# Optimization experiments

Hardware: AMD Instinct MI355X
Metric: run time of the kernel (lower is better)

## Reference

```python
import jax, jax.numpy as jnp
import numpy as np

N_ENT, N_USR, N_ITEM, N_REL, N_CLS, N_FAC, D = 100000, 4096, 8192, 32, 3, 8, 128
N_EDGES, NNZ = 800000, 204800


def setup_inputs() -> dict:
    key = jax.random.key(0)
    ks = jax.random.split(key, 15)
    return {
        "entity_emb": jax.random.normal(ks[0], (N_ENT, D), jnp.float32),
        "item_emb": jax.random.normal(ks[1], (N_ITEM, D), jnp.float32),
        "user_emb": jax.random.normal(ks[2], (N_USR, D), jnp.float32),
        "latent_emb": jax.random.normal(ks[3], (N_FAC, D), jnp.float32),
        "relation_emb": jax.random.normal(ks[4], (N_REL, D), jnp.float32),
        "edge_index": jax.random.randint(ks[5], (2, N_EDGES), 0, N_ENT, jnp.int32),
        "edge_type": jax.random.randint(ks[6], (N_EDGES,), 0, N_REL, jnp.int32),
        "edge_imp": jax.random.uniform(ks[7], (N_EDGES,), jnp.float32),
        "inter_rows": jax.random.randint(ks[8], (NNZ,), 0, N_USR, jnp.int32),
        "inter_cols": jax.random.randint(ks[9], (NNZ,), 0, N_ENT, jnp.int32),
        "inter_vals": jax.random.uniform(ks[10], (NNZ,), jnp.float32),
        "disen_weight_att": jax.random.normal(ks[11], (N_FAC, N_REL), jnp.float32),
        "ent_rel_w": jax.random.normal(ks[12], (N_REL, D), jnp.float32),
        "usr_cls_w": jax.random.normal(ks[13], (N_CLS, D), jnp.float32),
        "inter_cls_mat": jax.random.normal(ks[14], (N_CLS, N_USR, N_ITEM), jnp.float32),
    }


def reference(entity_emb, item_emb, user_emb, latent_emb, relation_emb,
              edge_index, edge_type, edge_imp, inter_rows, inter_cols,
              inter_vals, disen_weight_att, ent_rel_w, usr_cls_w, inter_cls_mat):
    n_entities = entity_emb.shape[0]
    n_users = user_emb.shape[0]
    head, tail = edge_index[0], edge_index[1]

    # --- entity aggregation, e_mode='att_imp' ---
    # per-entity attention over relations: [n_ent, n_rel]
    ent_rel_att = jax.nn.softmax(entity_emb @ relation_emb.T, axis=1)
    mess_att = ent_rel_att[head, edge_type][:, None]              # [E,1]
    message_score = relation_emb[edge_type] * mess_att * edge_imp[:, None]  # [E,D]
    message = entity_emb[tail] * message_score                    # [E,D]
    entity_agg = jax.ops.segment_sum(message, head, num_segments=n_entities)

    # --- user aggregation, u_mode='inter_cls' ---
    # sparse interact_mat @ entity_emb via COO gather + segment_sum
    user_agg = jax.ops.segment_sum(entity_emb[inter_cols] * inter_vals[:, None],
                                   inter_rows, num_segments=n_users)
    user_cls_att = jax.nn.softmax(user_emb @ usr_cls_w.T, axis=1)  # [U,C]
    item_emb_2 = item_emb * relation_emb.sum(axis=0, keepdims=True)  # [I,D]
    # stack_c(inter_cls_mat[c] @ item_emb_2).transpose(0,1) -> [U,C,D]
    disen_weight = jnp.einsum('cui,id->ucd', inter_cls_mat, item_emb_2)
    user_agg = user_agg + (disen_weight * user_cls_att[:, :, None]).sum(axis=1)

    return entity_agg, user_agg
```

## Files before the change

kernel.cpp:

```cpp
#include <hip/hip_runtime.h>

#define N_ENT   100000
#define N_USR   4096
#define N_ITEM  8192
#define N_REL   32
#define N_CLS   3
#define DD      128
#define N_EDGES 800000
#define NNZ     204800

#define CAP_E   64
#define CAP_U   128

typedef __attribute__((ext_vector_type(8))) short short8;
typedef __attribute__((ext_vector_type(4))) float f32x4;

static __device__ __forceinline__ unsigned short f2bf(float x) {
    unsigned int u = __builtin_bit_cast(unsigned int, x);
    u = (u + 0x7fffu + ((u >> 16) & 1u)) >> 16;
    return (unsigned short)u;
}
static __device__ __forceinline__ float bflo(unsigned int v) {
    return __uint_as_float(v << 16);
}
static __device__ __forceinline__ float bfhi(unsigned int v) {
    return __uint_as_float(v & 0xffff0000u);
}

#define ZB  ((N_ENT + N_USR + 255) / 256)
#define EAB ((N_ENT + 255) / 256)

__global__ __launch_bounds__(256) void k_prep(const float* __restrict__ ent,
                                              const float* __restrict__ rel,
                                              float* __restrict__ att,
                                              unsigned short* __restrict__ entbf,
                                              unsigned short* __restrict__ relbf,
                                              int* __restrict__ cnt,
                                              const float* __restrict__ item,
                                              unsigned short* __restrict__ Bt,
                                              const float* __restrict__ usr,
                                              const float* __restrict__ w,
                                              float* __restrict__ uatt) {
    __shared__ float smem[N_REL * DD];
    int bx = blockIdx.x;

    if (bx < ZB) {
        int i = bx * 256 + threadIdx.x;
        if (i < N_ENT + N_USR) cnt[i] = 0;
        return;
    }
    bx -= ZB;

    if (bx < EAB) {
        for (int i = threadIdx.x; i < N_REL * DD; i += 256) smem[i] = rel[i];
        __syncthreads();
        if (bx == 0) {
            for (int i = threadIdx.x; i < N_REL * DD; i += 256)
                relbf[i] = f2bf(smem[i]);
        }
        int e = bx * 256 + threadIdx.x;
        if (e >= N_ENT) return;
        const float4* row = (const float4*)(ent + (size_t)e * DD);
        unsigned short* brow = entbf + (size_t)e * DD;
        float acc[N_REL];
#pragma unroll
        for (int r = 0; r < N_REL; ++r) acc[r] = 0.f;
        for (int dq = 0; dq < DD / 4; ++dq) {
            float4 v = row[dq];
            ushort4 bv;
            bv.x = f2bf(v.x); bv.y = f2bf(v.y); bv.z = f2bf(v.z); bv.w = f2bf(v.w);
            *(ushort4*)(brow + dq * 4) = bv;
#pragma unroll
            for (int r = 0; r < N_REL; ++r) {
                float4 ww = *(const float4*)&smem[r * DD + dq * 4];
                acc[r] += v.x * ww.x + v.y * ww.y + v.z * ww.z + v.w * ww.w;
            }
        }
        float m = acc[0];
#pragma unroll
        for (int r = 1; r < N_REL; ++r) m = fmaxf(m, acc[r]);
        float s = 0.f;
#pragma unroll
        for (int r = 0; r < N_REL; ++r) { acc[r] = __expf(acc[r] - m); s += acc[r]; }
        float inv = 1.f / s;
        float* o = att + (size_t)e * N_REL;
#pragma unroll
        for (int r = 0; r < N_REL; ++r) o[r] = acc[r] * inv;
        return;
    }
    bx -= EAB;

    if (bx < 1024) {
        float (*tile)[33] = (float(*)[33])smem;
        float* ssum = smem + 32 * 33;
        const int b2 = bx & 255, by = bx >> 8;
        const int tx = threadIdx.x & 31, ty = threadIdx.x >> 5;
        const int i0 = b2 * 32, d0 = by * 32;
        if (threadIdx.x < 32) {
            float s = 0.f;
            for (int r = 0; r < N_REL; ++r) s += rel[r * DD + d0 + threadIdx.x];
            ssum[threadIdx.x] = s;
        }
#pragma unroll
        for (int rr = 0; rr < 4; ++rr)
            tile[ty + 8 * rr][tx] = item[(size_t)(i0 + ty + 8 * rr) * DD + d0 + tx];
        __syncthreads();
#pragma unroll
        for (int rr = 0; rr < 4; ++rr) {
            int d = d0 + ty + 8 * rr;
            Bt[(size_t)d * N_ITEM + i0 + tx] = f2bf(tile[tx][ty + 8 * rr] * ssum[ty + 8 * rr]);
        }
        return;
    }
    bx -= 1024;

    {
        for (int i = threadIdx.x; i < N_CLS * DD; i += 256) smem[i] = w[i];
        __syncthreads();
        int u = bx * 256 + threadIdx.x;
        const float4* row = (const float4*)(usr + (size_t)u * DD);
        float acc[3] = {0.f, 0.f, 0.f};
        for (int dq = 0; dq < DD / 4; ++dq) {
            float4 v = row[dq];
#pragma unroll
            for (int c = 0; c < 3; ++c) {
                float4 ww = *(const float4*)&smem[c * DD + dq * 4];
                acc[c] += v.x * ww.x + v.y * ww.y + v.z * ww.z + v.w * ww.w;
            }
        }
        float m = fmaxf(acc[0], fmaxf(acc[1], acc[2]));
        float s = 0.f;
#pragma unroll
        for (int c = 0; c < 3; ++c) { acc[c] = __expf(acc[c] - m); s += acc[c]; }
        float inv = 1.f / s;
#pragma unroll
        for (int c = 0; c < 3; ++c) uatt[u * 3 + c] = acc[c] * inv;
    }
}

#define BM 64
#define BK 32
#define SPLITK 16
#define KCH (N_ITEM / SPLITK)
#define PLANE ((long long)N_USR * N_ITEM)
#define GEMM_BLOCKS ((N_USR / BM) * SPLITK)
#define SCAT_BLOCKS ((N_EDGES + 255) / 256)

__global__ __launch_bounds__(256) void k_node2(const float* __restrict__ icm,
                                               const unsigned short* __restrict__ Bt,
                                               const float* __restrict__ uatt,
                                               float* __restrict__ part,
                                               const int* __restrict__ eidx,
                                               const int* __restrict__ etyp,
                                               const float* __restrict__ eimp,
                                               const int* __restrict__ irow,
                                               const int* __restrict__ icol,
                                               const float* __restrict__ ival,
                                               int* __restrict__ cnt,
                                               int2* __restrict__ pack_e,
                                               int2* __restrict__ pack_u) {
    __shared__ unsigned short smem[BM * 40 + DD * 40];

    if (blockIdx.x < GEMM_BLOCKS) {
        unsigned short (*sA)[40] = (unsigned short(*)[40])smem;
        unsigned short (*sB)[40] = (unsigned short(*)[40])(smem + BM * 40);

        const int t  = threadIdx.x;
        const int m0 = (blockIdx.x & 63) * BM;
        const int ky = blockIdx.x >> 6;
        const long long k0b = (long long)ky * KCH;

        const int ua = t >> 3;
        const int qa = t & 7;
        const float a00 = uatt[(m0 + ua) * 3 + 0];
        const float a01 = uatt[(m0 + ua) * 3 + 1];
        const float a02 = uatt[(m0 + ua) * 3 + 2];
        const float a10 = uatt[(m0 + ua + 32) * 3 + 0];
        const float a11 = uatt[(m0 + ua + 32) * 3 + 1];
        const float a12 = uatt[(m0 + ua + 32) * 3 + 2];

        const int db = t >> 2;
        const int qb = t & 3;

        const int lane = t & 63;
        const int wv = t >> 6;
        const int wm = wv >> 1, wn = wv & 1;
        const int la = lane & 15, lb = lane >> 4;

        f32x4 acc[2][4];
#pragma unroll
        for (int mi = 0; mi < 2; ++mi)
#pragma unroll
            for (int ni = 0; ni < 4; ++ni) {
                f32x4 z = {0.f, 0.f, 0.f, 0.f};
                acc[mi][ni] = z;
            }

        float4 rA0[3], rA1[3];
        short8 rB0, rB1;
        {
            const long long base0 = (long long)(m0 + ua) * N_ITEM + k0b + qa * 4;
            rA0[0] = *(const float4*)(icm + base0);
            rA0[1] = *(const float4*)(icm + base0 + PLANE);
            rA0[2] = *(const float4*)(icm + base0 + 2 * PLANE);
            const long long base1 = base0 + 32ll * N_ITEM;
            rA1[0] = *(const float4*)(icm + base1);
            rA1[1] = *(const float4*)(icm + base1 + PLANE);
            rA1[2] = *(const float4*)(icm + base1 + 2 * PLANE);
            const unsigned short* g0 = Bt + (long long)db * N_ITEM + k0b + qb * 8;
            rB0 = *(const short8*)g0;
            rB1 = *(const short8*)(g0 + 64ll * N_ITEM);
        }

        for (int kk = 0; kk < KCH; kk += BK) {
            __syncthreads();
            {
                ushort4 p;
                p.x = f2bf(a00 * rA0[0].x + a01 * rA0[1].x + a02 * rA0[2].x);
                p.y = f2bf(a00 * rA0[0].y + a01 * rA0[1].y + a02 * rA0[2].y);
                p.z = f2bf(a00 * rA0[0].z + a01 * rA0[1].z + a02 * rA0[2].z);
                p.w = f2bf(a00 * rA0[0].w + a01 * rA0[1].w + a02 * rA0[2].w);
                *(ushort4*)(&sA[ua][0] + qa * 4) = p;
                p.x = f2bf(a10 * rA1[0].x + a11 * rA1[1].x + a12 * rA1[2].x);
                p.y = f2bf(a10 * rA1[0].y + a11 * rA1[1].y + a12 * rA1[2].y);
                p.z = f2bf(a10 * rA1[0].z + a11 * rA1[1].z + a12 * rA1[2].z);
                p.w = f2bf(a10 * rA1[0].w + a11 * rA1[1].w + a12 * rA1[2].w);
                *(ushort4*)(&sA[ua + 32][0] + qa * 4) = p;
                *(short8*)(&sB[db][0] + qb * 8) = rB0;
                *(short8*)(&sB[db + 64][0] + qb * 8) = rB1;
            }
            __syncthreads();

            if (kk + BK < KCH) {
                const long long k0 = k0b + kk + BK;
                const long long base0 = (long long)(m0 + ua) * N_ITEM + k0 + qa * 4;
                rA0[0] = *(const float4*)(icm + base0);
                rA0[1] = *(const float4*)(icm + base0 + PLANE);
                rA0[2] = *(const float4*)(icm + base0 + 2 * PLANE);
                const long long base1 = base0 + 32ll * N_ITEM;
                rA1[0] = *(const float4*)(icm + base1);
                rA1[1] = *(const float4*)(icm + base1 + PLANE);
                rA1[2] = *(const float4*)(icm + base1 + 2 * PLANE);
                const unsigned short* g0 = Bt + (long long)db * N_ITEM + k0 + qb * 8;
                rB0 = *(const short8*)g0;
                rB1 = *(const short8*)(g0 + 64ll * N_ITEM);
            }

            short8 af[2], bfr[4];
#pragma unroll
            for (int mi = 0; mi < 2; ++mi)
                af[mi] = *(const short8*)(&sA[wm * 32 + mi * 16 + la][0] + lb * 8);
#pragma unroll
            for (int ni = 0; ni < 4; ++ni)
                bfr[ni] = *(const short8*)(&sB[wn * 64 + ni * 16 + la][0] + lb * 8);
#pragma unroll
            for (int mi = 0; mi < 2; ++mi)
#pragma unroll
                for (int ni = 0; ni < 4; ++ni)
                    acc[mi][ni] = __builtin_amdgcn_mfma_f32_16x16x32_bf16(
                        af[mi], bfr[ni], acc[mi][ni], 0, 0, 0);
        }

        float* pbase = part + (size_t)ky * ((size_t)N_USR * DD);
#pragma unroll
        for (int mi = 0; mi < 2; ++mi)
#pragma unroll
            for (int ni = 0; ni < 4; ++ni)
#pragma unroll
                for (int r = 0; r < 4; ++r) {
                    int row = m0 + wm * 32 + mi * 16 + lb * 4 + r;
                    int col = wn * 64 + ni * 16 + la;
                    pbase[(size_t)row * DD + col] = acc[mi][ni][r];
                }
    } else {
        int i = (blockIdx.x - GEMM_BLOCKS) * 256 + threadIdx.x;
        if (i < N_EDGES) {
            int h = eidx[i], tl = eidx[N_EDGES + i], r = etyp[i];
            int p = atomicAdd(&cnt[h], 1);
            if (p < CAP_E) {
                int2 pk;
                pk.x = tl | (r << 24);
                pk.y = __float_as_int(eimp[i]);
                pack_e[(size_t)h * CAP_E + p] = pk;
            }
        }
        if (i < NNZ) {
            int u = irow[i];
            int p = atomicAdd(&cnt[N_ENT + u], 1);
            if (p < CAP_U) {
                int2 pk;
                pk.x = icol[i];
                pk.y = __float_as_int(ival[i]);
                pack_u[(size_t)u * CAP_U + p] = pk;
            }
        }
    }
}

#define EDGE_BLOCKS (N_ENT / 16)
#define USER_BLOCKS (N_USR / 4)

__global__ __launch_bounds__(256) void k_node3(const unsigned short* __restrict__ entbf,
                                               const unsigned short* __restrict__ relbf,
                                               const float* __restrict__ att,
                                               const int2* __restrict__ pack_e,
                                               const int2* __restrict__ pack_u,
                                               const int* __restrict__ cnt,
                                               const float* __restrict__ part,
                                               float* __restrict__ out_ent,
                                               float* __restrict__ out_usr) {
    const int lane = threadIdx.x & 63;

    if (blockIdx.x < EDGE_BLOCKS) {
        const int wid = blockIdx.x * 4 + (threadIdx.x >> 6);
#pragma unroll
        for (int hh = 0; hh < 4; ++hh) {
            const int h = wid * 4 + hh;
            const int n = min(cnt[h], CAP_E);
            const float attv = att[(size_t)h * N_REL + (lane & 31)];
            const int2* seg = pack_e + (size_t)h * CAP_E;
            float ax = 0.f, ay = 0.f;
            for (int j = 0; j < n; j += 8) {
                int2 pk[8];
#pragma unroll
                for (int k = 0; k < 8; ++k) pk[k] = seg[min(j + k, n - 1)];
                unsigned int bv[8], rv[8];
                float sc[8];
#pragma unroll
                for (int k = 0; k < 8; ++k) {
                    int r = ((unsigned)pk[k].x) >> 24;
                    float s = __shfl(attv, r, 64) * __int_as_float(pk[k].y);
                    sc[k] = (j + k < n) ? s : 0.f;
                    bv[k] = ((const unsigned int*)(entbf + (size_t)(pk[k].x & 0xFFFFFF) * DD))[lane];
                    rv[k] = ((const unsigned int*)(relbf + (size_t)r * DD))[lane];
                }
#pragma unroll
                for (int k = 0; k < 8; ++k) {
                    ax = fmaf(bflo(rv[k]) * bflo(bv[k]), sc[k], ax);
                    ay = fmaf(bfhi(rv[k]) * bfhi(bv[k]), sc[k], ay);
                }
            }
            float2 o; o.x = ax; o.y = ay;
            ((float2*)(out_ent + (size_t)h * DD))[lane] = o;
        }
    } else {
        const int u = (blockIdx.x - EDGE_BLOCKS) * 4 + (threadIdx.x >> 6);
        const int n = min(cnt[N_ENT + u], CAP_U);
        const int2* seg = pack_u + (size_t)u * CAP_U;
        float ax = 0.f, ay = 0.f;
        for (int j = 0; j < n; j += 8) {
            int2 pk[8];
#pragma unroll
            for (int k = 0; k < 8; ++k) pk[k] = seg[min(j + k, n - 1)];
            unsigned int bv[8];
            float sc[8];
#pragma unroll
            for (int k = 0; k < 8; ++k) {
                sc[k] = (j + k < n) ? __int_as_float(pk[k].y) : 0.f;
                bv[k] = ((const unsigned int*)(entbf + (size_t)pk[k].x * DD))[lane];
            }
#pragma unroll
            for (int k = 0; k < 8; ++k) {
                ax = fmaf(bflo(bv[k]), sc[k], ax);
                ay = fmaf(bfhi(bv[k]), sc[k], ay);
            }
        }
#pragma unroll
        for (int k = 0; k < SPLITK; ++k) {
            float2 p = ((const float2*)(part + (size_t)k * N_USR * DD + (size_t)u * DD))[lane];
            ax += p.x;
            ay += p.y;
        }
        float2 o; o.x = ax; o.y = ay;
        ((float2*)(out_usr + (size_t)u * DD))[lane] = o;
    }
}

static constexpr size_t algn(size_t x) { return (x + 255) & ~(size_t)255; }

extern "C" void kernel_launch(void* const* d_in, const int* in_sizes, int n_in,
                              void* d_out, int out_size, void* d_ws, size_t ws_size,
                              hipStream_t stream) {
    const float* ent  = (const float*)d_in[0];
    const float* item = (const float*)d_in[1];
    const float* usr  = (const float*)d_in[2];
    const float* rel  = (const float*)d_in[4];
    const int*   eidx = (const int*)d_in[5];
    const int*   etyp = (const int*)d_in[6];
    const float* eimp = (const float*)d_in[7];
    const int*   irow = (const int*)d_in[8];
    const int*   icol = (const int*)d_in[9];
    const float* ival = (const float*)d_in[10];
    const float* uclw = (const float*)d_in[13];
    const float* icm  = (const float*)d_in[14];

    float* out_ent = (float*)d_out;
    float* out_usr = out_ent + (size_t)N_ENT * DD;

    char* w = (char*)d_ws;
    size_t o = 0;
    float* ws_att  = (float*)(w + o);  o = algn(o + (size_t)N_ENT * N_REL * 4);
    float* ws_uatt = (float*)(w + o);  o = algn(o + (size_t)N_USR * N_CLS * 4);
    unsigned short* ws_Bt    = (unsigned short*)(w + o); o = algn(o + (size_t)DD * N_ITEM * 2);
    unsigned short* ws_entbf = (unsigned short*)(w + o); o = algn(o + (size_t)N_ENT * DD * 2);
    unsigned short* ws_relbf = (unsigned short*)(w + o); o = algn(o + (size_t)N_REL * DD * 2);
    int*  ws_cnt   = (int*)(w + o);  o = algn(o + (size_t)(N_ENT + N_USR) * 4);
    int2* pack_e   = (int2*)(w + o); o = algn(o + (size_t)N_ENT * CAP_E * 8);
    int2* pack_u   = (int2*)(w + o); o = algn(o + (size_t)N_USR * CAP_U * 8);
    float* part    = (float*)(w + o); o = algn(o + (size_t)SPLITK * N_USR * DD * 4);

    (void)in_sizes; (void)n_in; (void)ws_size; (void)out_size;

    k_prep<<<ZB + EAB + 1024 + 16, 256, 0, stream>>>(ent, rel, ws_att, ws_entbf, ws_relbf,
                                                     ws_cnt, item, ws_Bt, usr, uclw, ws_uatt);
    k_node2<<<GEMM_BLOCKS + SCAT_BLOCKS, 256, 0, stream>>>(icm, ws_Bt, ws_uatt, part,
                                                           eidx, etyp, eimp, irow, icol, ival,
                                                           ws_cnt, pack_e, pack_u);
    k_node3<<<EDGE_BLOCKS + USER_BLOCKS, 256, 0, stream>>>(ws_entbf, ws_relbf, ws_att,
                                                           pack_e, pack_u, ws_cnt, part,
                                                           out_ent, out_usr);
}
```

Baseline: 313.8 us.

## Move entity attention prep into GEMM kernel and vectorize edge gather

The per-entity relation-softmax and bf16 conversion blocks move from the prep kernel into the GEMM/scatter kernel. They now run concurrently with the memory-bound split-K GEMM instead of ahead of it, which shortens the serial prep stage. The edge aggregation in k_node3 is also restructured so each 16-lane group loads 16-byte chunks of two edges per step, and partial sums are reduced across groups with xor shuffles. The shared-memory footprint of k_node2 grows to 16KB, which may reduce GEMM block occupancy.

```diff
diff --git a/kernel.cpp b/kernel.cpp
--- a/kernel.cpp
+++ b/kernel.cpp
@@ -28,20 +28,15 @@
 }
 
 #define ZB  ((N_ENT + N_USR + 255) / 256)
-#define EAB ((N_ENT + 255) / 256)
-
-__global__ __launch_bounds__(256) void k_prep(const float* __restrict__ ent,
-                                              const float* __restrict__ rel,
-                                              float* __restrict__ att,
-                                              unsigned short* __restrict__ entbf,
-                                              unsigned short* __restrict__ relbf,
-                                              int* __restrict__ cnt,
-                                              const float* __restrict__ item,
-                                              unsigned short* __restrict__ Bt,
-                                              const float* __restrict__ usr,
-                                              const float* __restrict__ w,
-                                              float* __restrict__ uatt) {
-    __shared__ float smem[N_REL * DD];
+
+__global__ __launch_bounds__(256) void k_prep_light(const float* __restrict__ rel,
+                                                    int* __restrict__ cnt,
+                                                    const float* __restrict__ item,
+                                                    unsigned short* __restrict__ Bt,
+                                                    const float* __restrict__ usr,
+                                                    const float* __restrict__ w,
+                                                    float* __restrict__ uatt) {
+    __shared__ float smem[32 * 33 + 32];
     int bx = blockIdx.x;
 
     if (bx < ZB) {
@@ -50,45 +45,6 @@
         return;
     }
     bx -= ZB;
-
-    if (bx < EAB) {
-        for (int i = threadIdx.x; i < N_REL * DD; i += 256) smem[i] = rel[i];
-        __syncthreads();
-        if (bx == 0) {
-            for (int i = threadIdx.x; i < N_REL * DD; i += 256)
-                relbf[i] = f2bf(smem[i]);
-        }
-        int e = bx * 256 + threadIdx.x;
-        if (e >= N_ENT) return;
-        const float4* row = (const float4*)(ent + (size_t)e * DD);
-        unsigned short* brow = entbf + (size_t)e * DD;
-        float acc[N_REL];
-#pragma unroll
-        for (int r = 0; r < N_REL; ++r) acc[r] = 0.f;
-        for (int dq = 0; dq < DD / 4; ++dq) {
-            float4 v = row[dq];
-            ushort4 bv;
-            bv.x = f2bf(v.x); bv.y = f2bf(v.y); bv.z = f2bf(v.z); bv.w = f2bf(v.w);
-            *(ushort4*)(brow + dq * 4) = bv;
-#pragma unroll
-            for (int r = 0; r < N_REL; ++r) {
-                float4 ww = *(const float4*)&smem[r * DD + dq * 4];
-                acc[r] += v.x * ww.x + v.y * ww.y + v.z * ww.z + v.w * ww.w;
-            }
-        }
-        float m = acc[0];
-#pragma unroll
-        for (int r = 1; r < N_REL; ++r) m = fmaxf(m, acc[r]);
-        float s = 0.f;
-#pragma unroll
-        for (int r = 0; r < N_REL; ++r) { acc[r] = __expf(acc[r] - m); s += acc[r]; }
-        float inv = 1.f / s;
-        float* o = att + (size_t)e * N_REL;
-#pragma unroll
-        for (int r = 0; r < N_REL; ++r) o[r] = acc[r] * inv;
-        return;
-    }
-    bx -= EAB;
 
     if (bx < 1024) {
         float (*tile)[33] = (float(*)[33])smem;
@@ -144,12 +100,18 @@
 #define KCH (N_ITEM / SPLITK)
 #define PLANE ((long long)N_USR * N_ITEM)
 #define GEMM_BLOCKS ((N_USR / BM) * SPLITK)
+#define EAB ((N_ENT + 255) / 256)
 #define SCAT_BLOCKS ((N_EDGES + 255) / 256)
 
 __global__ __launch_bounds__(256) void k_node2(const float* __restrict__ icm,
                                                const unsigned short* __restrict__ Bt,
                                                const float* __restrict__ uatt,
                                                float* __restrict__ part,
+                                               const float* __restrict__ ent,
+                                               const float* __restrict__ rel,
+                                               float* __restrict__ att,
+                                               unsigned short* __restrict__ entbf,
+                                               unsigned short* __restrict__ relbf,
                                                const int* __restrict__ eidx,
                                                const int* __restrict__ etyp,
                                                const float* __restrict__ eimp,
@@ -159,9 +121,10 @@
                                                int* __restrict__ cnt,
                                                int2* __restrict__ pack_e,
                                                int2* __restrict__ pack_u) {
-    __shared__ unsigned short smem[BM * 40 + DD * 40];
+    __shared__ float smemf[N_REL * DD];
 
     if (blockIdx.x < GEMM_BLOCKS) {
+        unsigned short* smem = (unsigned short*)smemf;
         unsigned short (*sA)[40] = (unsigned short(*)[40])smem;
         unsigned short (*sB)[40] = (unsigned short(*)[40])(smem + BM * 40);
 
@@ -272,8 +235,50 @@
                     int col = wn * 64 + ni * 16 + la;
                     pbase[(size_t)row * DD + col] = acc[mi][ni][r];
                 }
-    } else {
-        int i = (blockIdx.x - GEMM_BLOCKS) * 256 + threadIdx.x;
+        return;
+    }
+
+    if (blockIdx.x < GEMM_BLOCKS + EAB) {
+        int bx = blockIdx.x - GEMM_BLOCKS;
+        for (int i = threadIdx.x; i < N_REL * DD; i += 256) smemf[i] = rel[i];
+        __syncthreads();
+        if (bx == 0) {
+            for (int i = threadIdx.x; i < N_REL * DD; i += 256)
+                relbf[i] = f2bf(smemf[i]);
+        }
+        int e = bx * 256 + threadIdx.x;
+        if (e >= N_ENT) return;
+        const float4* row = (const float4*)(ent + (size_t)e * DD);
+        unsigned short* brow = entbf + (size_t)e * DD;
+        float acc[N_REL];
+#pragma unroll
+        for (int r = 0; r < N_REL; ++r) acc[r] = 0.f;
+        for (int dq = 0; dq < DD / 4; ++dq) {
+            float4 v = row[dq];
+            ushort4 bv;
+            bv.x = f2bf(v.x); bv.y = f2bf(v.y); bv.z = f2bf(v.z); bv.w = f2bf(v.w);
+            *(ushort4*)(brow + dq * 4) = bv;
+#pragma unroll
+            for (int r = 0; r < N_REL; ++r) {
+                float4 ww = *(const float4*)&smemf[r * DD + dq * 4];
+                acc[r] += v.x * ww.x + v.y * ww.y + v.z * ww.z + v.w * ww.w;
+            }
+        }
+        float m = acc[0];
+#pragma unroll
+        for (int r = 1; r < N_REL; ++r) m = fmaxf(m, acc[r]);
+        float s = 0.f;
+#pragma unroll
+        for (int r = 0; r < N_REL; ++r) { acc[r] = __expf(acc[r] - m); s += acc[r]; }
+        float inv = 1.f / s;
+        float* o = att + (size_t)e * N_REL;
+#pragma unroll
+        for (int r = 0; r < N_REL; ++r) o[r] = acc[r] * inv;
+        return;
+    }
+
+    {
+        int i = (blockIdx.x - GEMM_BLOCKS - EAB) * 256 + threadIdx.x;
         if (i < N_EDGES) {
             int h = eidx[i], tl = eidx[N_EDGES + i], r = etyp[i];
             int p = atomicAdd(&cnt[h], 1);
@@ -313,35 +318,55 @@
 
     if (blockIdx.x < EDGE_BLOCKS) {
         const int wid = blockIdx.x * 4 + (threadIdx.x >> 6);
-#pragma unroll
+        const int l15 = lane & 15;
+        const int grp = lane >> 4;
+#pragma unroll 1
         for (int hh = 0; hh < 4; ++hh) {
             const int h = wid * 4 + hh;
             const int n = min(cnt[h], CAP_E);
             const float attv = att[(size_t)h * N_REL + (lane & 31)];
             const int2* seg = pack_e + (size_t)h * CAP_E;
-            float ax = 0.f, ay = 0.f;
+            float acc[8];
+#pragma unroll
+            for (int e = 0; e < 8; ++e) acc[e] = 0.f;
             for (int j = 0; j < n; j += 8) {
-                int2 pk[8];
-#pragma unroll
-                for (int k = 0; k < 8; ++k) pk[k] = seg[min(j + k, n - 1)];
-                unsigned int bv[8], rv[8];
-                float sc[8];
-#pragma unroll
-                for (int k = 0; k < 8; ++k) {
-                    int r = ((unsigned)pk[k].x) >> 24;
-                    float s = __shfl(attv, r, 64) * __int_as_float(pk[k].y);
-                    sc[k] = (j + k < n) ? s : 0.f;
-                    bv[k] = ((const unsigned int*)(entbf + (size_t)(pk[k].x & 0xFFFFFF) * DD))[lane];
-                    rv[k] = ((const unsigned int*)(relbf + (size_t)r * DD))[lane];
+                const int e0 = j + grp, e1 = j + 4 + grp;
+                int2 p0 = seg[min(e0, n - 1)];
+                int2 p1 = seg[min(e1, n - 1)];
+                const int r0 = ((unsigned)p0.x) >> 24;
+                const int r1 = ((unsigned)p1.x) >> 24;
+                float s0 = __shfl(attv, r0, 64) * __int_as_float(p0.y);
+                float s1 = __shfl(attv, r1, 64) * __int_as_float(p1.y);
+                s0 = (e0 < n) ? s0 : 0.f;
+                s1 = (e1 < n) ? s1 : 0.f;
+                uint4 b0 = ((const uint4*)(entbf + (size_t)(p0.x & 0xFFFFFF) * DD))[l15];
+                uint4 b1 = ((const uint4*)(entbf + (size_t)(p1.x & 0xFFFFFF) * DD))[l15];
+                uint4 v0 = ((const uint4*)(relbf + (size_t)r0 * DD))[l15];
+                uint4 v1 = ((const uint4*)(relbf + (size_t)r1 * DD))[l15];
+                const unsigned* bp0 = (const unsigned*)&b0;
+                const unsigned* bp1 = (const unsigned*)&b1;
+                const unsigned* vp0 = (const unsigned*)&v0;
+                const unsigned* vp1 = (const unsigned*)&v1;
+#pragma unroll
+                for (int q = 0; q < 4; ++q) {
+                    acc[2 * q]     = fmaf(bflo(bp0[q]) * bflo(vp0[q]), s0, acc[2 * q]);
+                    acc[2 * q + 1] = fmaf(bfhi(bp0[q]) * bfhi(vp0[q]), s0, acc[2 * q + 1]);
+                    acc[2 * q]     = fmaf(bflo(bp1[q]) * bflo(vp1[q]), s1, acc[2 * q]);
+                    acc[2 * q + 1] = fmaf(bfhi(bp1[q]) * bfhi(vp1[q]), s1, acc[2 * q + 1]);
                 }
-#pragma unroll
-                for (int k = 0; k < 8; ++k) {
-                    ax = fmaf(bflo(rv[k]) * bflo(bv[k]), sc[k], ax);
-                    ay = fmaf(bfhi(rv[k]) * bfhi(bv[k]), sc[k], ay);
-                }
-            }
-            float2 o; o.x = ax; o.y = ay;
-            ((float2*)(out_ent + (size_t)h * DD))[lane] = o;
+            }
+#pragma unroll
+            for (int e = 0; e < 8; ++e) {
+                acc[e] += __shfl_xor(acc[e], 16, 64);
+                acc[e] += __shfl_xor(acc[e], 32, 64);
+            }
+            if (lane < 16) {
+                float4 o0 = {acc[0], acc[1], acc[2], acc[3]};
+                float4 o1 = {acc[4], acc[5], acc[6], acc[7]};
+                float4* dst = (float4*)(out_ent + (size_t)h * DD) + l15 * 2;
+                dst[0] = o0;
+                dst[1] = o1;
+            }
         }
     } else {
         const int u = (blockIdx.x - EDGE_BLOCKS) * 4 + (threadIdx.x >> 6);
@@ -411,11 +436,11 @@
 
     (void)in_sizes; (void)n_in; (void)ws_size; (void)out_size;
 
-    k_prep<<<ZB + EAB + 1024 + 16, 256, 0, stream>>>(ent, rel, ws_att, ws_entbf, ws_relbf,
-                                                     ws_cnt, item, ws_Bt, usr, uclw, ws_uatt);
-    k_node2<<<GEMM_BLOCKS + SCAT_BLOCKS, 256, 0, stream>>>(icm, ws_Bt, ws_uatt, part,
-                                                           eidx, etyp, eimp, irow, icol, ival,
-                                                           ws_cnt, pack_e, pack_u);
+    k_prep_light<<<ZB + 1024 + 16, 256, 0, stream>>>(rel, ws_cnt, item, ws_Bt,
+                                                     usr, uclw, ws_uatt);
+    k_node2<<<GEMM_BLOCKS + EAB + SCAT_BLOCKS, 256, 0, stream>>>(
+        icm, ws_Bt, ws_uatt, part, ent, rel, ws_att, ws_entbf, ws_relbf,
+        eidx, etyp, eimp, irow, icol, ival, ws_cnt, pack_e, pack_u);
     k_node3<<<EDGE_BLOCKS + USER_BLOCKS, 256, 0, stream>>>(ws_entbf, ws_relbf, ws_att,
                                                            pack_e, pack_u, ws_cnt, part,
                                                            out_ent, out_usr);
```

Measured after the change: 268.4 us. 14.5% less time.
